# Kernel optimization log

Hardware: AMD Instinct MI355X
Metric: run time of the kernel (lower is better)

## Reference

```python
import jax, jax.numpy as jnp
import numpy as np

F, H, E, D, B = 1024, 256, 64, 64, 4096
N = F + H


def setup_inputs() -> dict:
    key = jax.random.key(0)
    k = jax.random.split(key, 7)
    values = jax.random.normal(k[0], (B, F), dtype=jnp.float32)
    # GlorotNormal-ish init for embeddings and dense layers
    feat_emb = jax.random.normal(k[1], (F, E), dtype=jnp.float32) * (2.0 / (F + E)) ** 0.5
    hidden_emb = jax.random.normal(k[2], (H, E), dtype=jnp.float32) * (2.0 / (H + E)) ** 0.5
    w_kernel = jax.random.normal(k[3], (2 * E, D), dtype=jnp.float32) * (2.0 / (2 * E + D)) ** 0.5
    w_bias = jnp.zeros((D,), dtype=jnp.float32)
    u_kernel = jax.random.normal(k[4], (D,), dtype=jnp.float32) * (2.0 / (D + 1)) ** 0.5
    # sparse ancestor mask; every node is its own ancestor -> diagonal True
    mask = jax.random.bernoulli(k[5], 0.02, (F, N))
    mask = mask.at[jnp.arange(F), jnp.arange(F)].set(True)
    return {
        "values": values,
        "feat_emb": feat_emb,
        "hidden_emb": hidden_emb,
        "w_kernel": w_kernel,
        "w_bias": w_bias,
        "u_kernel": u_kernel,
        "mask": mask,
    }


def reference(values, feat_emb, hidden_emb, w_kernel, w_bias, u_kernel, mask):
    # full embedding table: [N, E]
    full = jnp.concatenate([feat_emb, hidden_emb], axis=0)
    # Dense(w) applied to concat([e_i, f_j]) == e_i @ Wa + f_j @ Wb + b
    Wa, Wb = w_kernel[:E], w_kernel[E:]
    feat_proj = feat_emb @ Wa            # [F, D]
    full_proj = full @ Wb                # [N, D]
    h = jnp.tanh(feat_proj[:, None, :] + full_proj[None, :, :] + w_bias)  # [F, N, D]
    score = jnp.einsum("fnd,d->fn", h, u_kernel)  # [F, N]
    # masked exp / normalize (faithful to tf.where(mask, exp(score), 0) / sum)
    escore = jnp.where(mask, jnp.exp(score), 0.0)
    attn = escore / jnp.sum(escore, axis=1, keepdims=True)  # [F, N]
    context = attn @ full                # [F, E]
    return values @ context              # [B, E]
```

## Files before the change

kernel.cpp:

```cpp
#include <hip/hip_runtime.h>
#include <stdint.h>

#define F 1024
#define H 256
#define E 64
#define D 64
#define B 4096
#define NN 1280

typedef __attribute__((ext_vector_type(8))) short bf16x8;
typedef __attribute__((ext_vector_type(4))) float f32x4;

__device__ inline uint16_t f2bf_rne(float x) {
    union { float f; uint32_t u; } v; v.f = x;
    uint32_t u = v.u + 0x7fffu + ((v.u >> 16) & 1u);
    return (uint16_t)(u >> 16);
}
__device__ inline float bf2f(uint16_t h) {
    union { uint32_t u; float f; } v; v.u = ((uint32_t)h) << 16;
    return v.f;
}

__device__ void probe_mask_body(const void* __restrict__ mask, int* __restrict__ flag) {
    __shared__ int s_byte, s_int, s_float;
    int t = threadIdx.x;
    if (t == 0) { s_byte = 1; s_int = 1; s_float = 1; }
    __syncthreads();
    long idx = (long)t * NN + t;
    const uint8_t* mb = (const uint8_t*)mask;
    const int*     mi = (const int*)mask;
    const float*   mf = (const float*)mask;
    if (mb[idx] != 1)    atomicAnd(&s_byte, 0);
    if (mi[idx] != 1)    atomicAnd(&s_int, 0);
    if (mf[idx] != 1.0f) atomicAnd(&s_float, 0);
    __syncthreads();
    if (t == 0) {
        int mode = 0;
        if (s_byte) mode = 0;
        else if (s_int) mode = 1;
        else if (s_float) mode = 2;
        flag[0] = mode;
    }
}

__global__ void proj_kernel(const float* __restrict__ feat_emb,
                            const float* __restrict__ hidden_emb,
                            const float* __restrict__ w_kernel,
                            const void*  __restrict__ mask,
                            float* __restrict__ fp, float* __restrict__ gp,
                            int* __restrict__ flag) {
    if (blockIdx.x == (F + NN) / 4) {
        probe_mask_body(mask, flag);
        return;
    }
    int tid = threadIdx.x;
    int r = blockIdx.x * 4 + (tid >> 6);
    int d = tid & 63;
    const float* emb;
    const float* W;
    float* outp;
    if (r < F) {
        emb = feat_emb + (size_t)r * E;
        W = w_kernel;
        outp = fp + (size_t)r * D + d;
    } else {
        int rn = r - F;
        emb = (rn < F) ? (feat_emb + (size_t)rn * E)
                       : (hidden_emb + (size_t)(rn - F) * E);
        W = w_kernel + (size_t)E * D;
        outp = gp + (size_t)rn * D + d;
    }
    float acc = 0.f;
#pragma unroll
    for (int e = 0; e < E; ++e) acc = fmaf(emb[e], W[e * D + d], acc);
    *outp = acc;
}

__global__ __launch_bounds__(256)
void attn_ctx_kernel(const float* __restrict__ feat_emb,
                     const float* __restrict__ hidden_emb,
                     const void*  __restrict__ mask,
                     const float* __restrict__ w_bias,
                     const float* __restrict__ u_kernel,
                     const float* __restrict__ fp,
                     const float* __restrict__ gp,
                     const int*   __restrict__ flag,
                     uint16_t* __restrict__ ctxB_hi,
                     uint16_t* __restrict__ ctxB_lo) {
    __shared__ float s_cacc[4][64];
    __shared__ float s_den[4];
    int tid = threadIdx.x;
    int w = tid >> 6, lane = tid & 63;
    int f = blockIdx.x;
    int mode = flag[0];
    float uk  = u_kernel[lane];
    float bv  = w_bias[lane];
    float fpv = fp[(size_t)f * D + lane];
    float denom = 0.f, cacc = 0.f;
    const uint8_t* mb = (const uint8_t*)mask;
    const int*     mi = (const int*)mask;
    const float*   mf = (const float*)mask;
    for (int nb = w * 320; nb < w * 320 + 320; nb += 64) {
        long midx = (long)f * NN + nb + lane;
        bool mv;
        if (mode == 0)      mv = (mb[midx] != 0);
        else if (mode == 1) mv = (mi[midx] != 0);
        else                mv = (mf[midx] != 0.f);
        unsigned long long bal = __ballot(mv);
        while (bal) {
            int bit = __ffsll(bal) - 1;
            bal &= bal - 1;
            int n = nb + bit;
            float gpv = gp[(size_t)n * D + lane];
            float t = uk * tanhf(fpv + gpv + bv);
#pragma unroll
            for (int off = 32; off; off >>= 1) t += __shfl_xor(t, off);
            float es = expf(t);
            denom += es;
            float fullv = (n < F) ? feat_emb[(size_t)n * E + lane]
                                  : hidden_emb[(size_t)(n - F) * E + lane];
            cacc = fmaf(es, fullv, cacc);
        }
    }
    s_cacc[w][lane] = cacc;
    if (lane == 0) s_den[w] = denom;
    __syncthreads();
    if (w == 0) {
        float c = s_cacc[0][lane] + s_cacc[1][lane] + s_cacc[2][lane] + s_cacc[3][lane];
        float dn = s_den[0] + s_den[1] + s_den[2] + s_den[3];
        c /= dn;
        uint16_t hi = f2bf_rne(c);
        float lof = c - bf2f(hi);
        uint16_t lo = f2bf_rne(lof);
        int ks = f >> 5, kk = f & 31;
        int ch = kk >> 3, j = kk & 7;
        int l  = ch * 16 + (lane & 15);
        int nt = lane >> 4;
        int off = ((ks * 4 + nt) * 64 + l) * 8 + j;
        ctxB_hi[off] = hi;
        ctxB_lo[off] = lo;
    }
}

#define OKW 16
__global__ __launch_bounds__(1024, 4)
void out_kernel(const float* __restrict__ values,
                const uint16_t* __restrict__ ctxB_hi,
                const uint16_t* __restrict__ ctxB_lo,
                float* __restrict__ out) {
    __shared__ float red[OKW][16][64];
    int tid = threadIdx.x;
    int w = tid >> 6, l = tid & 63;
    int m0 = blockIdx.x * 16;
    f32x4 acc[4];
#pragma unroll
    for (int nt = 0; nt < 4; ++nt) acc[nt] = (f32x4){0.f, 0.f, 0.f, 0.f};
    int row = m0 + (l & 15);
    int kchunk = (l >> 4) * 8;
#pragma unroll
    for (int s = 0; s < 2; ++s) {
        int ks = w * 2 + s;
        int k0 = ks * 32 + kchunk;
        const float4 va0 = *reinterpret_cast<const float4*>(values + (size_t)row * F + k0);
        const float4 va1 = *reinterpret_cast<const float4*>(values + (size_t)row * F + k0 + 4);
        float av0 = va0.x, av1 = va0.y, av2 = va0.z, av3 = va0.w;
        float av4 = va1.x, av5 = va1.y, av6 = va1.z, av7 = va1.w;
        bf16x8 ahi, alo;
        {
            uint16_t h;
            h = f2bf_rne(av0); ahi[0] = (short)h; alo[0] = (short)f2bf_rne(av0 - bf2f(h));
            h = f2bf_rne(av1); ahi[1] = (short)h; alo[1] = (short)f2bf_rne(av1 - bf2f(h));
            h = f2bf_rne(av2); ahi[2] = (short)h; alo[2] = (short)f2bf_rne(av2 - bf2f(h));
            h = f2bf_rne(av3); ahi[3] = (short)h; alo[3] = (short)f2bf_rne(av3 - bf2f(h));
            h = f2bf_rne(av4); ahi[4] = (short)h; alo[4] = (short)f2bf_rne(av4 - bf2f(h));
            h = f2bf_rne(av5); ahi[5] = (short)h; alo[5] = (short)f2bf_rne(av5 - bf2f(h));
            h = f2bf_rne(av6); ahi[6] = (short)h; alo[6] = (short)f2bf_rne(av6 - bf2f(h));
            h = f2bf_rne(av7); ahi[7] = (short)h; alo[7] = (short)f2bf_rne(av7 - bf2f(h));
        }
#pragma unroll
        for (int nt = 0; nt < 4; ++nt) {
            int boff = ((ks * 4 + nt) * 64 + l) * 8;
            bf16x8 bhi = *reinterpret_cast<const bf16x8*>(ctxB_hi + boff);
            bf16x8 blo = *reinterpret_cast<const bf16x8*>(ctxB_lo + boff);
            acc[nt] = __builtin_amdgcn_mfma_f32_16x16x32_bf16(ahi, bhi, acc[nt], 0, 0, 0);
            acc[nt] = __builtin_amdgcn_mfma_f32_16x16x32_bf16(ahi, blo, acc[nt], 0, 0, 0);
            acc[nt] = __builtin_amdgcn_mfma_f32_16x16x32_bf16(alo, bhi, acc[nt], 0, 0, 0);
        }
    }
#pragma unroll
    for (int nt = 0; nt < 4; ++nt)
#pragma unroll
        for (int r = 0; r < 4; ++r) {
            int orow = (l >> 4) * 4 + r;
            int ocol = nt * 16 + (l & 15);
            red[w][orow][ocol] = acc[nt][r];
        }
    __syncthreads();
    int orow = tid >> 6, ocol = tid & 63;
    float s2 = 0.f;
#pragma unroll
    for (int ww = 0; ww < OKW; ++ww) s2 += red[ww][orow][ocol];
    out[(size_t)(m0 + orow) * D + ocol] = s2;
}

extern "C" void kernel_launch(void* const* d_in, const int* in_sizes, int n_in,
                              void* d_out, int out_size, void* d_ws, size_t ws_size,
                              hipStream_t stream) {
    const float* values     = (const float*)d_in[0];
    const float* feat_emb   = (const float*)d_in[1];
    const float* hidden_emb = (const float*)d_in[2];
    const float* w_kernel   = (const float*)d_in[3];
    const float* w_bias     = (const float*)d_in[4];
    const float* u_kernel   = (const float*)d_in[5];
    const void*  mask       = (const void*)d_in[6];
    float* out = (float*)d_out;

    int*      flag    = (int*)d_ws;
    float*    wsf     = (float*)d_ws;
    float*    fp      = wsf + 64;
    float*    gp      = fp + F * D;
    uint16_t* ctxB_hi = (uint16_t*)(gp + NN * D);
    uint16_t* ctxB_lo = ctxB_hi + 32 * 4 * 64 * 8;

    proj_kernel<<<(F + NN) / 4 + 1, 256, 0, stream>>>(feat_emb, hidden_emb, w_kernel,
                                                      mask, fp, gp, flag);
    attn_ctx_kernel<<<F, 256, 0, stream>>>(feat_emb, hidden_emb, mask, w_bias,
                                           u_kernel, fp, gp, flag, ctxB_hi, ctxB_lo);
    out_kernel<<<B / 16, 1024, 0, stream>>>(values, ctxB_hi, ctxB_lo, out);
}
```

Measured before the change: 28.41 us.

## Compact mask indices in LDS and batch attention gathers with fast tanh

The attention kernel now loads all five mask chunks up front, compacts the active column indices into shared memory with ballot/popcount, and then handles them four at a time. This lets the gp and embedding gathers for four columns be issued together, overlapping their latencies instead of serialising one column per loop iteration. tanhf and expf are replaced with exp2-based approximations using a hardware reciprocal, which is cheaper but slightly less accurate. The projection kernel also splits its dot product into four accumulators to shorten the FMA dependency chain.

```diff
diff --git a/kernel.cpp b/kernel.cpp
--- a/kernel.cpp
+++ b/kernel.cpp
@@ -70,10 +70,15 @@
         W = w_kernel + (size_t)E * D;
         outp = gp + (size_t)rn * D + d;
     }
-    float acc = 0.f;
-#pragma unroll
-    for (int e = 0; e < E; ++e) acc = fmaf(emb[e], W[e * D + d], acc);
-    *outp = acc;
+    float a0 = 0.f, a1 = 0.f, a2 = 0.f, a3 = 0.f;
+#pragma unroll
+    for (int e = 0; e < E; e += 4) {
+        a0 = fmaf(emb[e + 0], W[(e + 0) * D + d], a0);
+        a1 = fmaf(emb[e + 1], W[(e + 1) * D + d], a1);
+        a2 = fmaf(emb[e + 2], W[(e + 2) * D + d], a2);
+        a3 = fmaf(emb[e + 3], W[(e + 3) * D + d], a3);
+    }
+    *outp = (a0 + a1) + (a2 + a3);
 }
 
 __global__ __launch_bounds__(256)
@@ -89,6 +94,7 @@
                      uint16_t* __restrict__ ctxB_lo) {
     __shared__ float s_cacc[4][64];
     __shared__ float s_den[4];
+    __shared__ unsigned short s_idx[4][320];
     int tid = threadIdx.x;
     int w = tid >> 6, lane = tid & 63;
     int f = blockIdx.x;
@@ -96,30 +102,64 @@
     float uk  = u_kernel[lane];
     float bv  = w_bias[lane];
     float fpv = fp[(size_t)f * D + lane];
-    float denom = 0.f, cacc = 0.f;
     const uint8_t* mb = (const uint8_t*)mask;
     const int*     mi = (const int*)mask;
     const float*   mf = (const float*)mask;
-    for (int nb = w * 320; nb < w * 320 + 320; nb += 64) {
-        long midx = (long)f * NN + nb + lane;
-        bool mv;
-        if (mode == 0)      mv = (mb[midx] != 0);
-        else if (mode == 1) mv = (mi[midx] != 0);
-        else                mv = (mf[midx] != 0.f);
-        unsigned long long bal = __ballot(mv);
-        while (bal) {
-            int bit = __ffsll(bal) - 1;
-            bal &= bal - 1;
-            int n = nb + bit;
-            float gpv = gp[(size_t)n * D + lane];
-            float t = uk * tanhf(fpv + gpv + bv);
+
+    bool mv[5];
+    long base = (long)f * NN + w * 320;
+#pragma unroll
+    for (int c = 0; c < 5; ++c) {
+        long midx = base + c * 64 + lane;
+        if (mode == 0)      mv[c] = (mb[midx] != 0);
+        else if (mode == 1) mv[c] = (mi[midx] != 0);
+        else                mv[c] = (mf[midx] != 0.f);
+    }
+    unsigned long long below = lane ? (~0ull >> (64 - lane)) : 0ull;
+    int cnt = 0;
+#pragma unroll
+    for (int c = 0; c < 5; ++c) {
+        unsigned long long bal = __ballot(mv[c]);
+        if (mv[c]) {
+            int pos = cnt + __popcll(bal & below);
+            s_idx[w][pos] = (unsigned short)(w * 320 + c * 64 + lane);
+        }
+        cnt += __popcll(bal);
+    }
+
+    float denom = 0.f, cacc = 0.f;
+    const float k2E = 2.885390082f;
+    const float kE  = 1.44269504f;
+    for (int i = 0; i < cnt; i += 4) {
+        int   n[4];
+        float g[4], fv[4];
+        bool  valid[4];
+#pragma unroll
+        for (int j = 0; j < 4; ++j) {
+            valid[j] = (i + j) < cnt;
+            n[j] = s_idx[w][valid[j] ? i + j : i];
+        }
+#pragma unroll
+        for (int j = 0; j < 4; ++j) g[j] = gp[(size_t)n[j] * D + lane];
+#pragma unroll
+        for (int j = 0; j < 4; ++j)
+            fv[j] = (n[j] < F) ? feat_emb[(size_t)n[j] * E + lane]
+                               : hidden_emb[(size_t)(n[j] - F) * E + lane];
+#pragma unroll
+        for (int j = 0; j < 4; ++j) {
+            float x  = fpv + g[j] + bv;
+            float ax = fminf(fabsf(x), 10.f);
+            float ex = exp2f(k2E * ax);
+            float th = (ex - 1.f) * __builtin_amdgcn_rcpf(ex + 1.f);
+            th = copysignf(th, x);
+            float t = uk * th;
 #pragma unroll
             for (int off = 32; off; off >>= 1) t += __shfl_xor(t, off);
-            float es = expf(t);
-            denom += es;
-            float fullv = (n < F) ? feat_emb[(size_t)n * E + lane]
-                                  : hidden_emb[(size_t)(n - F) * E + lane];
-            cacc = fmaf(es, fullv, cacc);
+            float es = exp2f(t * kE);
+            if (valid[j]) {
+                denom += es;
+                cacc = fmaf(es, fv[j], cacc);
+            }
         }
     }
     s_cacc[w][lane] = cacc;
```

Measured after the change: 25.26 us. -11.1%, faster.
